# Optimization experiments

Measured on AMD Instinct MI355X. Metric: run time of the kernel, lower is better.

The kernel has to match this reference:

```python
import jax, jax.numpy as jnp
import numpy as np

EMB_SIZE = 768
BLOCK_SIZE = 64
OFFSET = 1  # bert cls offset


def setup_inputs() -> dict:
    key = jax.random.key(0)
    ks = jax.random.split(key, 10)
    n, c, d, h, E, M, P = 4, 1024, 768, 12, 42, 8, 1024
    sequence_output = jax.random.normal(ks[0], (n, c, d), jnp.float32)
    attention = jax.random.uniform(ks[1], (n, h, c, c), jnp.float32)
    attention = attention / attention.sum(-1, keepdims=True)  # softmax-like rows
    Wh = jax.random.normal(ks[2], (EMB_SIZE, 2 * d), jnp.float32) * 0.02
    bh = jax.random.normal(ks[3], (EMB_SIZE,), jnp.float32) * 0.02
    Wt = jax.random.normal(ks[4], (EMB_SIZE, 2 * d), jnp.float32) * 0.02
    bt = jax.random.normal(ks[5], (EMB_SIZE,), jnp.float32) * 0.02
    Wb = jax.random.normal(ks[6], (99, EMB_SIZE * BLOCK_SIZE), jnp.float32) * 0.02
    mention_pos = jax.random.randint(ks[7], (n, E, M), 0, c - 1 - OFFSET, jnp.int32)
    mention_mask = jax.random.randint(ks[8], (n, E, M), 0, 2, jnp.int32)
    mention_mask = mention_mask.at[:, :, 0].set(1)  # every entity has >=1 mention
    hts = jax.random.randint(ks[9], (n, P, 2), 0, E, jnp.int32)
    return {"sequence_output": sequence_output, "attention": attention,
            "Wh": Wh, "bh": bh, "Wt": Wt, "bt": bt, "Wb": Wb,
            "mention_pos": mention_pos, "mention_mask": mention_mask, "hts": hts}


def _get_hrt_doc(seq, att, pos, mask, ht):
    # seq [c,d], att [h,c,c], pos/mask [E,M], ht [P,2]
    p = pos + OFFSET                                   # [E,M]
    valid = mask > 0
    memb = seq[p]                                      # [E,M,d] gather
    e_emb = jax.scipy.special.logsumexp(
        jnp.where(valid[..., None], memb, -jnp.inf), axis=1)  # [E,d]
    matt = att[:, p]                                   # [h,E,M,c] gather
    cnt = valid.sum(1).astype(seq.dtype)               # [E]
    e_att = (matt * valid[None, :, :, None].astype(seq.dtype)).sum(2)
    e_att = jnp.transpose(e_att, (1, 0, 2)) / cnt[:, None, None]  # [E,h,c] mention mean
    hs = e_emb[ht[:, 0]]                               # [P,d]
    ts = e_emb[ht[:, 1]]
    h_att = e_att[ht[:, 0]]                            # [P,h,c]
    t_att = e_att[ht[:, 1]]
    ht_att = (h_att * t_att).mean(1)                   # [P,c] head mean
    ht_att = ht_att / (ht_att.sum(1, keepdims=True) + 1e-5)
    rs = jnp.einsum('ld,rl->rd', seq, ht_att)          # [P,d]
    return hs, ts, rs


def reference(sequence_output, attention, Wh, bh, Wt, bt, Wb,
              mention_pos, mention_mask, hts):
    d = sequence_output.shape[-1]
    hs, ts, rs = jax.vmap(_get_hrt_doc)(sequence_output, attention,
                                        mention_pos, mention_mask, hts)
    hs = hs.reshape(-1, d)
    ts = ts.reshape(-1, d)
    rs = rs.reshape(-1, d)
    hs = jnp.tanh(jnp.concatenate([hs, rs], axis=1) @ Wh.T + bh)
    ts = jnp.tanh(jnp.concatenate([ts, rs], axis=1) @ Wt.T + bt)
    nb = EMB_SIZE // BLOCK_SIZE
    b1 = hs.reshape(-1, nb, BLOCK_SIZE)
    b2 = ts.reshape(-1, nb, BLOCK_SIZE)
    bl = (b1[:, :, :, None] * b2[:, :, None, :]).reshape(-1, EMB_SIZE * BLOCK_SIZE)
    logits = bl @ Wb.T                                 # [N, num_labels+2]
    return logits
```

## Files before the change

### kernel.cpp

```cpp
#include <hip/hip_runtime.h>
#include <hip/hip_bf16.h>
#include <hip/hip_fp16.h>
#include <math.h>

#define NDOC 4
#define CCC  1024
#define DDD  768
#define HHH  12
#define EEE  42
#define MMM  8
#define PPP  1024
#define NK   99
#define NPAD 112
#define NSLICE 96

typedef __attribute__((ext_vector_type(8))) short short8v;
typedef __attribute__((ext_vector_type(8))) _Float16 half8;
typedef __attribute__((ext_vector_type(4))) float floatx4;

__device__ __forceinline__ unsigned short f32_to_bf16u(float f) {
  return __builtin_bit_cast(unsigned short, __float2bfloat16(f));
}
__device__ __forceinline__ unsigned short f32_to_f16u(float f) {
  return __builtin_bit_cast(unsigned short, __float2half(f));
}

__global__ __launch_bounds__(256) void k_prep(
    const float* __restrict__ seq, const float* __restrict__ att,
    const float* __restrict__ Wh, const float* __restrict__ Wt,
    const float* __restrict__ Wb,
    const int* __restrict__ pos, const int* __restrict__ mask,
    unsigned short* __restrict__ eembB, float* __restrict__ eatt,
    unsigned short* __restrict__ WhtB, unsigned short* __restrict__ seqTB,
    unsigned short* __restrict__ WpB) {
  const int bx = blockIdx.x;
  const int tid = threadIdx.x;
  if (bx < 168) {
    int e = bx % EEE, doc = bx / EEE;
    int base = (doc*EEE + e)*MMM;
    int p[MMM], mk[MMM];
#pragma unroll
    for (int m = 0; m < MMM; ++m) { p[m] = pos[base+m] + 1; mk[m] = mask[base+m]; }
    for (int d0 = tid; d0 < DDD; d0 += 256) {
      float v[MMM]; float mx = -INFINITY;
#pragma unroll
      for (int m = 0; m < MMM; ++m) {
        v[m] = seq[(doc*CCC + p[m])*DDD + d0];
        if (mk[m]) mx = fmaxf(mx, v[m]);
      }
      float s = 0.f;
#pragma unroll
      for (int m = 0; m < MMM; ++m) if (mk[m]) s += expf(v[m]-mx);
      eembB[(doc*EEE + e)*DDD + d0] = f32_to_bf16u(logf(s) + mx);
    }
  } else if (bx < 2184) {
    int b = bx - 168;
    int head = b % HHH, e = (b/HHH) % EEE, doc = b / (HHH*EEE);
    int base = (doc*EEE + e)*MMM;
    int j = tid * 4;
    float ax=0.f, ay=0.f, az=0.f, aw=0.f; float cnt = 0.f;
#pragma unroll
    for (int m = 0; m < MMM; ++m) {
      int mk = mask[base+m];
      cnt += (float)mk;
      if (mk) {
        int pp = pos[base+m] + 1;
        const float4 a = *(const float4*)&att[((size_t)(doc*HHH + head)*CCC + pp)*CCC + j];
        ax += a.x; ay += a.y; az += a.z; aw += a.w;
      }
    }
    float inv = 1.f / cnt;
    float4 o; o.x = ax*inv; o.y = ay*inv; o.z = az*inv; o.w = aw*inv;
    *(float4*)&eatt[((size_t)((doc*EEE + e)*HHH + head))*CCC + j] = o;
  } else if (bx < 3336) {
    int gid = (bx - 2184)*256 + tid;
    int half = gid >= 147456;
    int loc = half ? gid - 147456 : gid;
    const float* src = (half ? Wt : Wh) + (size_t)loc*8;
    float4 v0 = *(const float4*)src;
    float4 v1 = *(const float4*)(src+4);
    unsigned short o[8];
    o[0]=f32_to_bf16u(v0.x); o[1]=f32_to_bf16u(v0.y); o[2]=f32_to_bf16u(v0.z); o[3]=f32_to_bf16u(v0.w);
    o[4]=f32_to_bf16u(v1.x); o[5]=f32_to_bf16u(v1.y); o[6]=f32_to_bf16u(v1.z); o[7]=f32_to_bf16u(v1.w);
    *(uint4*)&WhtB[(size_t)half*1179648 + (size_t)loc*8] = *(const uint4*)o;
  } else if (bx < 4104) {
    __shared__ float tl[64][65];
    int b = bx - 3336;
    int d0 = (b % 12)*64, c0 = ((b/12) % 16)*64, doc = b / 192;
#pragma unroll
    for (int rep = 0; rep < 4; ++rep) {
      int cr = rep*16 + (tid >> 4);
      int d4 = (tid & 15) * 4;
      float4 v = *(const float4*)&seq[((size_t)doc*CCC + c0 + cr)*DDD + d0 + d4];
      tl[cr][d4+0]=v.x; tl[cr][d4+1]=v.y; tl[cr][d4+2]=v.z; tl[cr][d4+3]=v.w;
    }
    __syncthreads();
#pragma unroll
    for (int rep = 0; rep < 4; ++rep) {
      int dr = rep*16 + (tid >> 4);
      int c4 = (tid & 15) * 4;
      unsigned short o[4];
#pragma unroll
      for (int kq = 0; kq < 4; ++kq)
        o[kq] = f32_to_bf16u(tl[c4+kq][dr]);
      *(uint2*)&seqTB[((size_t)doc*DDD + d0 + dr)*CCC + c0 + c4] = *(const uint2*)o;
    }
  } else {
    int t = (bx - 4104)*256 + tid;
    int n  = t / 6144;
    int rem = t % 6144;
    int ki = rem >> 3;
    int j8 = (rem & 7) * 8;
    unsigned short o[8];
    if (n < NK) {
      const float* src = &Wb[(size_t)n*49152 + ki*64 + j8];
      float4 v0 = *(const float4*)src;
      float4 v1 = *(const float4*)(src+4);
      o[0]=f32_to_f16u(v0.x); o[1]=f32_to_f16u(v0.y); o[2]=f32_to_f16u(v0.z); o[3]=f32_to_f16u(v0.w);
      o[4]=f32_to_f16u(v1.x); o[5]=f32_to_f16u(v1.y); o[6]=f32_to_f16u(v1.z); o[7]=f32_to_f16u(v1.w);
    } else {
#pragma unroll
      for (int e=0;e<8;++e) o[e]=0;
    }
    int js = j8 >> 5, q = (j8 >> 3) & 3;
    int nt = n >> 4, lnn = n & 15;
    int c = ((js*7 + nt)*4 + q)*16 + lnn;
    *(uint4*)&WpB[(size_t)ki*7168 + c*8] = *(const uint4*)o;
  }
}

__global__ __launch_bounds__(256) void k_htatt1(const float* __restrict__ eatt,
    const int* __restrict__ hts, float* __restrict__ htU,
    float* __restrict__ Ssum) {
  __shared__ float tile[EEE*16*12];
  const int cg = blockIdx.x, doc = blockIdx.y;
  const int c0 = cg * 16;
  for (int idx = threadIdx.x; idx < EEE*16*12; idx += 256) {
    int e = idx / 192, rem = idx % 192, h = rem / 16, cc = rem % 16;
    tile[(e*16 + cc)*12 + h] =
        eatt[((size_t)((doc*EEE + e)*HHH + h))*CCC + c0 + cc];
  }
  __syncthreads();
  const int cc = threadIdx.x & 15;
  const int pg = threadIdx.x >> 4;
  for (int it = 0; it < 64; ++it) {
    int p = pg + it*16;
    int h0 = hts[(doc*PPP + p)*2 + 0];
    int t0 = hts[(doc*PPP + p)*2 + 1];
    const float* a = &tile[(h0*16 + cc)*12];
    const float* b = &tile[(t0*16 + cc)*12];
    float4 a0 = *(const float4*)a,     b0 = *(const float4*)b;
    float4 a1 = *(const float4*)(a+4), b1 = *(const float4*)(b+4);
    float4 a2 = *(const float4*)(a+8), b2 = *(const float4*)(b+8);
    float s = a0.x*b0.x + a0.y*b0.y + a0.z*b0.z + a0.w*b0.w
            + a1.x*b1.x + a1.y*b1.y + a1.z*b1.z + a1.w*b1.w
            + a2.x*b2.x + a2.y*b2.y + a2.z*b2.z + a2.w*b2.w;
    s *= (1.f/12.f);
    htU[((size_t)(doc*PPP + p))*CCC + c0 + cc] = s;
    float r = s;
    r += __shfl_xor(r, 1, 16);
    r += __shfl_xor(r, 2, 16);
    r += __shfl_xor(r, 4, 16);
    r += __shfl_xor(r, 8, 16);
    if (cc == 0) Ssum[((size_t)(doc*PPP + p))*64 + cg] = r;
  }
}

__global__ __launch_bounds__(256) void k_htnorm(const float* __restrict__ htU,
    const float* __restrict__ Ssum, unsigned short* __restrict__ htB) {
  __shared__ float sc_sh;
  const int b = blockIdx.x;
  const int lane = threadIdx.x;
  if (lane < 64) {
    float r = Ssum[(size_t)b*64 + lane];
    for (int off = 32; off > 0; off >>= 1) r += __shfl_down(r, off, 64);
    if (lane == 0) sc_sh = 1.f / (r + 1e-5f);
  }
  __syncthreads();
  float sc = sc_sh;
  float4 v = *(const float4*)&htU[(size_t)b*CCC + lane*4];
  unsigned short o[4];
  o[0] = f32_to_bf16u(v.x*sc); o[1] = f32_to_bf16u(v.y*sc);
  o[2] = f32_to_bf16u(v.z*sc); o[3] = f32_to_bf16u(v.w*sc);
  *(uint2*)&htB[(size_t)b*CCC + lane*4] = *(const uint2*)o;
}

__global__ __launch_bounds__(256) void k_rs_mfma(
    const unsigned short* __restrict__ htB,
    const unsigned short* __restrict__ seqTB,
    unsigned short* __restrict__ rsB) {
  __shared__ unsigned short A_l[4096];
  __shared__ unsigned short B_l[4096];
  const int n0 = blockIdx.x * 128;
  const int m0 = blockIdx.y * 128;
  const int doc = m0 >> 10;
  const int mloc = m0 & 1023;
  const int t = threadIdx.x;
  const int lane = t & 63;
  const int ln = lane & 15, q4 = lane >> 4;
  const int w = t >> 6;
  const int wr = w >> 1, wc = w & 1;

  const int r0 = t >> 2;
  const int koff = (t & 3) * 8;
  const unsigned short* srcA0 = htB + ((size_t)doc*CCC + mloc + r0)*CCC + koff;
  const unsigned short* srcA1 = htB + ((size_t)doc*CCC + mloc + r0 + 64)*CCC + koff;
  const unsigned short* srcB0 = seqTB + ((size_t)doc*DDD + n0 + r0)*CCC + koff;
  const unsigned short* srcB1 = seqTB + ((size_t)doc*DDD + n0 + r0 + 64)*CCC + koff;

  floatx4 acc[4][4];
#pragma unroll
  for (int i = 0; i < 4; ++i)
#pragma unroll
    for (int j = 0; j < 4; ++j) acc[i][j] = (floatx4){0.f,0.f,0.f,0.f};

  for (int k0 = 0; k0 < CCC; k0 += 32) {
    uint4 va0 = *(const uint4*)(srcA0 + k0);
    uint4 va1 = *(const uint4*)(srcA1 + k0);
    uint4 vb0 = *(const uint4*)(srcB0 + k0);
    uint4 vb1 = *(const uint4*)(srcB1 + k0);
    __syncthreads();
    *(uint4*)&A_l[(size_t)t*8]       = va0;
    *(uint4*)&A_l[(size_t)(t+256)*8] = va1;
    *(uint4*)&B_l[(size_t)t*8]       = vb0;
    *(uint4*)&B_l[(size_t)(t+256)*8] = vb1;
    __syncthreads();
    short8v a[4], b[4];
#pragma unroll
    for (int rt = 0; rt < 4; ++rt)
      a[rt] = *(const short8v*)&A_l[((wr*64 + rt*16 + ln)*4 + q4)*8];
#pragma unroll
    for (int nt = 0; nt < 4; ++nt)
      b[nt] = *(const short8v*)&B_l[((wc*64 + nt*16 + ln)*4 + q4)*8];
#pragma unroll
    for (int rt = 0; rt < 4; ++rt)
#pragma unroll
      for (int nt = 0; nt < 4; ++nt)
        acc[rt][nt] = __builtin_amdgcn_mfma_f32_16x16x32_bf16(a[rt], b[nt], acc[rt][nt], 0, 0, 0);
  }
#pragma unroll
  for (int rt = 0; rt < 4; ++rt)
#pragma unroll
    for (int nt = 0; nt < 4; ++nt) {
      int col = n0 + wc*64 + nt*16 + ln;
#pragma unroll
      for (int reg = 0; reg < 4; ++reg) {
        int row = m0 + wr*64 + rt*16 + q4*4 + reg;
        rsB[(size_t)row*DDD + col] = f32_to_bf16u(acc[rt][nt][reg]);
      }
    }
}

__global__ __launch_bounds__(256) void k_heads_mfma(
    const unsigned short* __restrict__ eembB,
    const unsigned short* __restrict__ rsB,
    const int* __restrict__ hts,
    const unsigned short* __restrict__ WB,
    const float* __restrict__ bh, const float* __restrict__ bt,
    unsigned short* __restrict__ hsTB,
    unsigned short* __restrict__ tsbH) {
  __shared__ unsigned short A_l[4096];
  __shared__ unsigned short B_l[4096];
  __shared__ unsigned short T_l[128*144];
  const int which = blockIdx.z;
  const int n0 = blockIdx.x * 128;
  const int m0 = blockIdx.y * 128;
  const int doc = m0 >> 10;
  const int t = threadIdx.x;
  const int lane = t & 63;
  const int ln = lane & 15, q4 = lane >> 4;
  const int w = t >> 6;
  const int wr = w >> 1, wc = w & 1;

  const int r0 = t >> 2;
  const int koff = (t & 3) * 8;
  const int rgA0 = m0 + r0, rgA1 = m0 + r0 + 64;
  const int idx0 = hts[rgA0*2 + which];
  const int idx1 = hts[rgA1*2 + which];
  const unsigned short* srcE0 = eembB + (size_t)(doc*EEE + idx0)*DDD + koff;
  const unsigned short* srcE1 = eembB + (size_t)(doc*EEE + idx1)*DDD + koff;
  const unsigned short* srcR0 = rsB + (size_t)rgA0*DDD + koff;
  const unsigned short* srcR1 = rsB + (size_t)rgA1*DDD + koff;
  const unsigned short* WBz = WB + (size_t)which*1179648;
  const unsigned short* srcW0 = WBz + (size_t)(n0 + r0)*1536 + koff;
  const unsigned short* srcW1 = WBz + (size_t)(n0 + r0 + 64)*1536 + koff;

  floatx4 acc[4][4];
#pragma unroll
  for (int i = 0; i < 4; ++i)
#pragma unroll
    for (int j = 0; j < 4; ++j) acc[i][j] = (floatx4){0.f,0.f,0.f,0.f};

  for (int k0 = 0; k0 < 1536; k0 += 32) {
    uint4 va0 = (k0 < DDD) ? *(const uint4*)(srcE0 + k0) : *(const uint4*)(srcR0 + (k0 - DDD));
    uint4 va1 = (k0 < DDD) ? *(const uint4*)(srcE1 + k0) : *(const uint4*)(srcR1 + (k0 - DDD));
    uint4 vb0 = *(const uint4*)(srcW0 + k0);
    uint4 vb1 = *(const uint4*)(srcW1 + k0);
    __syncthreads();
    *(uint4*)&A_l[(size_t)t*8]       = va0;
    *(uint4*)&A_l[(size_t)(t+256)*8] = va1;
    *(uint4*)&B_l[(size_t)t*8]       = vb0;
    *(uint4*)&B_l[(size_t)(t+256)*8] = vb1;
    __syncthreads();
    short8v a[4], b[4];
#pragma unroll
    for (int rt = 0; rt < 4; ++rt)
      a[rt] = *(const short8v*)&A_l[((wr*64 + rt*16 + ln)*4 + q4)*8];
#pragma unroll
    for (int nt = 0; nt < 4; ++nt)
      b[nt] = *(const short8v*)&B_l[((wc*64 + nt*16 + ln)*4 + q4)*8];
#pragma unroll
    for (int rt = 0; rt < 4; ++rt)
#pragma unroll
      for (int nt = 0; nt < 4; ++nt)
        acc[rt][nt] = __builtin_amdgcn_mfma_f32_16x16x32_bf16(a[rt], b[nt], acc[rt][nt], 0, 0, 0);
  }
  const float* bias = which ? bt : bh;
  if (which == 0) {
#pragma unroll
    for (int rt = 0; rt < 4; ++rt)
#pragma unroll
      for (int nt = 0; nt < 4; ++nt) {
        int col = wc*64 + nt*16 + ln;
        float bsv = bias[n0 + col];
#pragma unroll
        for (int reg = 0; reg < 4; ++reg) {
          int row = wr*64 + rt*16 + q4*4 + reg;
          T_l[col*144 + row] = f32_to_f16u(tanhf(acc[rt][nt][reg] + bsv));
        }
      }
    __syncthreads();
#pragma unroll
    for (int iter = 0; iter < 8; ++iter) {
      int col = iter*16 + (t >> 4);
      int rblk = t & 15;
      uint4 v = *(const uint4*)&T_l[col*144 + rblk*8];
      *(uint4*)&hsTB[(size_t)(n0 + col)*4096 + m0 + rblk*8] = v;
    }
  } else {
#pragma unroll
    for (int rt = 0; rt < 4; ++rt)
#pragma unroll
      for (int nt = 0; nt < 4; ++nt) {
        int col = n0 + wc*64 + nt*16 + ln;
        float bsv = bias[col];
#pragma unroll
        for (int reg = 0; reg < 4; ++reg) {
          int row = m0 + wr*64 + rt*16 + q4*4 + reg;
          tsbH[(size_t)row*DDD + col] = f32_to_f16u(tanhf(acc[rt][nt][reg] + bsv));
        }
      }
  }
}

__global__ __launch_bounds__(128) void k_logits_mfma(
    const unsigned short* __restrict__ hsT,
    const unsigned short* __restrict__ tsbH,
    const unsigned short* __restrict__ Wp,
    unsigned short* __restrict__ P) {
  __shared__ unsigned short hsT_l[8*128];
  const int slice = blockIdx.x;
  const int kbase = slice * 8;
  const int nb = slice >> 3;
  const int mtile = blockIdx.y;
  const int t = threadIdx.x;
  const int w = t >> 6;
  const int lane = t & 63;
  const int ln = lane & 15;
  const int q = lane >> 4;
  const int m0w = mtile*128 + w*64;

  {
    int ii = t >> 4;
    int c8 = (t & 15) * 8;
    uint4 v = *(const uint4*)&hsT[(size_t)(kbase + ii)*4096 + mtile*128 + c8];
    *(uint4*)&hsT_l[ii*128 + c8] = v;
  }

  __half2 tsr2[4][2][4];
#pragma unroll
  for (int rt = 0; rt < 4; ++rt) {
    int row = m0w + rt*16 + ln;
#pragma unroll
    for (int js = 0; js < 2; ++js) {
      uint4 v = *(const uint4*)&tsbH[(size_t)row*DDD + nb*64 + js*32 + q*8];
      tsr2[rt][js][0] = __builtin_bit_cast(__half2, v.x);
      tsr2[rt][js][1] = __builtin_bit_cast(__half2, v.y);
      tsr2[rt][js][2] = __builtin_bit_cast(__half2, v.z);
      tsr2[rt][js][3] = __builtin_bit_cast(__half2, v.w);
    }
  }

  floatx4 acc[4][7];
#pragma unroll
  for (int rt = 0; rt < 4; ++rt)
#pragma unroll
    for (int nt = 0; nt < 7; ++nt)
      acc[rt][nt] = (floatx4){0.f,0.f,0.f,0.f};

  __syncthreads();

  const unsigned short* wb = Wp + (size_t)kbase*7168;
#pragma unroll
  for (int ii = 0; ii < 8; ++ii) {
    __half2 hh[4];
#pragma unroll
    for (int rt = 0; rt < 4; ++rt) {
      unsigned short hb = hsT_l[ii*128 + w*64 + rt*16 + ln];
      hh[rt] = __half2half2(__ushort_as_half(hb));
    }
#pragma unroll
    for (int js = 0; js < 2; ++js) {
      half8 b[7];
#pragma unroll
      for (int nt = 0; nt < 7; ++nt)
        b[nt] = __builtin_bit_cast(half8,
            *(const uint4*)&wb[((size_t)ii*896 + (js*7 + nt)*64 + lane)*8]);
      half8 a[4];
#pragma unroll
      for (int rt = 0; rt < 4; ++rt) {
        uint4 au;
        au.x = __builtin_bit_cast(unsigned int, __hmul2(hh[rt], tsr2[rt][js][0]));
        au.y = __builtin_bit_cast(unsigned int, __hmul2(hh[rt], tsr2[rt][js][1]));
        au.z = __builtin_bit_cast(unsigned int, __hmul2(hh[rt], tsr2[rt][js][2]));
        au.w = __builtin_bit_cast(unsigned int, __hmul2(hh[rt], tsr2[rt][js][3]));
        a[rt] = __builtin_bit_cast(half8, au);
      }
#pragma unroll
      for (int nt = 0; nt < 7; ++nt)
#pragma unroll
        for (int rt = 0; rt < 4; ++rt)
          acc[rt][nt] = __builtin_amdgcn_mfma_f32_16x16x32_f16(a[rt], b[nt], acc[rt][nt], 0, 0, 0);
    }
  }

  unsigned short* Ps = P + (size_t)slice*(4096*NPAD);
#pragma unroll
  for (int nt = 0; nt < 7; ++nt) {
    int col = nt*16 + ln;
#pragma unroll
    for (int rt = 0; rt < 4; ++rt) {
#pragma unroll
      for (int reg = 0; reg < 4; ++reg) {
        int row = m0w + rt*16 + q*4 + reg;
        Ps[(size_t)row*NPAD + col] = f32_to_f16u(acc[rt][nt][reg]);
      }
    }
  }
}

__global__ __launch_bounds__(256) void k_logred(const unsigned short* __restrict__ P,
    float* __restrict__ out) {
  int idx = blockIdx.x*256 + threadIdx.x;
  int r = idx / NPAD;
  int c = idx % NPAD;
  if (c >= NK) return;
  float s = 0.f;
#pragma unroll 8
  for (int sl = 0; sl < NSLICE; ++sl)
    s += __half2float(__ushort_as_half(P[(size_t)sl*(4096*NPAD) + idx]));
  out[(size_t)r*NK + c] = s;
}

extern "C" void kernel_launch(void* const* d_in, const int* in_sizes, int n_in,
                              void* d_out, int out_size, void* d_ws, size_t ws_size,
                              hipStream_t stream) {
  const float* seq  = (const float*)d_in[0];
  const float* att  = (const float*)d_in[1];
  const float* Wh   = (const float*)d_in[2];
  const float* bh   = (const float*)d_in[3];
  const float* Wt   = (const float*)d_in[4];
  const float* bt   = (const float*)d_in[5];
  const float* Wb   = (const float*)d_in[6];
  const int* pos    = (const int*)d_in[7];
  const int* mask   = (const int*)d_in[8];
  const int* hts    = (const int*)d_in[9];
  float* out = (float*)d_out;

  float* ws = (float*)d_ws;
  float*          eatt  = ws;
  float*          htU   = ws + 2064384;
  float*          Ssum  = ws + 6258688;
  unsigned short* htB   = (unsigned short*)(ws + 6520832);
  unsigned short* eembB = (unsigned short*)(ws + 8617984);
  unsigned short* seqTB = (unsigned short*)(ws + 8682496);
  unsigned short* WhtB  = (unsigned short*)(ws + 10255360);
  unsigned short* rsB   = (unsigned short*)(ws + 11435008);
  unsigned short* hsTB  = (unsigned short*)(ws + 13007872);
  unsigned short* tsbH  = (unsigned short*)(ws + 14580736);
  unsigned short* WpB   = (unsigned short*)(ws + 16153600);
  unsigned short* Pp    = (unsigned short*)(ws + 18906112);

  k_prep<<<dim3(6792), 256, 0, stream>>>(seq, att, Wh, Wt, Wb, pos, mask,
                                         eembB, eatt, WhtB, seqTB, WpB);
  k_htatt1<<<dim3(64, NDOC), 256, 0, stream>>>(eatt, hts, htU, Ssum);
  k_htnorm<<<dim3(NDOC*PPP), 256, 0, stream>>>(htU, Ssum, htB);
  k_rs_mfma<<<dim3(6, 32), 256, 0, stream>>>(htB, seqTB, rsB);
  k_heads_mfma<<<dim3(6, 32, 2), 256, 0, stream>>>(eembB, rsB, hts, WhtB, bh, bt, hsTB, tsbH);
  k_logits_mfma<<<dim3(NSLICE, 32), 128, 0, stream>>>(hsTB, tsbH, WpB, Pp);
  k_logred<<<dim3(4096*NPAD/256), 256, 0, stream>>>(Pp, out);
}
```

Measured before the change: 257.8 us.

## Restructure logits kernel: larger tiles, LDS-staged weights with register prefetch, XCD swizzle

The logits MFMA kernel now has each 256-thread block cover 256 rows and 16 k-slices, halving the slice count and the partial-sum traffic into the reduction. Weight tiles are staged cooperatively into shared memory, with the next tile prefetched into registers while the current one is used. Block indices are remapped so neighbouring work groups land on the same XCD. Partial outputs are written with nontemporal stores. The costs are extra barriers, more register pressure and more LDS use per block.

```diff
diff --git a/kernel.cpp b/kernel.cpp
--- a/kernel.cpp
+++ b/kernel.cpp
@@ -12,7 +12,7 @@
 #define PPP  1024
 #define NK   99
 #define NPAD 112
-#define NSLICE 96
+#define NSLICE 48
 
 typedef __attribute__((ext_vector_type(8))) short short8v;
 typedef __attribute__((ext_vector_type(8))) _Float16 half8;
@@ -353,28 +353,33 @@
   }
 }
 
-__global__ __launch_bounds__(128) void k_logits_mfma(
+__global__ __launch_bounds__(256) void k_logits_mfma(
     const unsigned short* __restrict__ hsT,
     const unsigned short* __restrict__ tsbH,
     const unsigned short* __restrict__ Wp,
     unsigned short* __restrict__ P) {
-  __shared__ unsigned short hsT_l[8*128];
-  const int slice = blockIdx.x;
-  const int kbase = slice * 8;
-  const int nb = slice >> 3;
-  const int mtile = blockIdx.y;
+  __shared__ unsigned short hsT_l[16*256];
+  __shared__ unsigned short slab[2*7168];
+  const int bid = blockIdx.x;
+  const int wg = (bid & 7)*96 + (bid >> 3);
+  const int slice = wg >> 4;
+  const int mgroup = wg & 15;
+  const int kbase = slice * 16;
+  const int nb = kbase >> 6;
   const int t = threadIdx.x;
   const int w = t >> 6;
   const int lane = t & 63;
   const int ln = lane & 15;
   const int q = lane >> 4;
-  const int m0w = mtile*128 + w*64;
-
-  {
-    int ii = t >> 4;
-    int c8 = (t & 15) * 8;
-    uint4 v = *(const uint4*)&hsT[(size_t)(kbase + ii)*4096 + mtile*128 + c8];
-    *(uint4*)&hsT_l[ii*128 + c8] = v;
+  const int m0w = mgroup*256 + w*64;
+
+#pragma unroll
+  for (int rep = 0; rep < 2; ++rep) {
+    int c16 = t + rep*256;
+    int ii = c16 >> 5;
+    int c8 = (c16 & 31) * 8;
+    uint4 v = *(const uint4*)&hsT[(size_t)(kbase + ii)*4096 + mgroup*256 + c8];
+    *(uint4*)&hsT_l[ii*256 + c8] = v;
   }
 
   __half2 tsr2[4][2][4];
@@ -398,39 +403,61 @@
     for (int nt = 0; nt < 7; ++nt)
       acc[rt][nt] = (floatx4){0.f,0.f,0.f,0.f};
 
+  uint4 wreg[7];
+#pragma unroll
+  for (int r = 0; r < 7; ++r)
+    wreg[r] = *(const uint4*)&Wp[(size_t)kbase*7168 + (t + r*256)*8];
+#pragma unroll
+  for (int r = 0; r < 7; ++r)
+    *(uint4*)&slab[(t + r*256)*8] = wreg[r];
   __syncthreads();
 
-  const unsigned short* wb = Wp + (size_t)kbase*7168;
-#pragma unroll
-  for (int ii = 0; ii < 8; ++ii) {
-    __half2 hh[4];
-#pragma unroll
-    for (int rt = 0; rt < 4; ++rt) {
-      unsigned short hb = hsT_l[ii*128 + w*64 + rt*16 + ln];
-      hh[rt] = __half2half2(__ushort_as_half(hb));
-    }
-#pragma unroll
-    for (int js = 0; js < 2; ++js) {
-      half8 b[7];
-#pragma unroll
-      for (int nt = 0; nt < 7; ++nt)
-        b[nt] = __builtin_bit_cast(half8,
-            *(const uint4*)&wb[((size_t)ii*896 + (js*7 + nt)*64 + lane)*8]);
-      half8 a[4];
+  for (int ks = 0; ks < 8; ++ks) {
+    if (ks < 7) {
+      int kin = kbase + (ks + 1)*2;
+#pragma unroll
+      for (int r = 0; r < 7; ++r)
+        wreg[r] = *(const uint4*)&Wp[(size_t)kin*7168 + (t + r*256)*8];
+    }
+#pragma unroll
+    for (int il = 0; il < 2; ++il) {
+      int ii = ks*2 + il;
+      __half2 hh[4];
 #pragma unroll
       for (int rt = 0; rt < 4; ++rt) {
-        uint4 au;
-        au.x = __builtin_bit_cast(unsigned int, __hmul2(hh[rt], tsr2[rt][js][0]));
-        au.y = __builtin_bit_cast(unsigned int, __hmul2(hh[rt], tsr2[rt][js][1]));
-        au.z = __builtin_bit_cast(unsigned int, __hmul2(hh[rt], tsr2[rt][js][2]));
-        au.w = __builtin_bit_cast(unsigned int, __hmul2(hh[rt], tsr2[rt][js][3]));
-        a[rt] = __builtin_bit_cast(half8, au);
-      }
-#pragma unroll
-      for (int nt = 0; nt < 7; ++nt)
-#pragma unroll
-        for (int rt = 0; rt < 4; ++rt)
-          acc[rt][nt] = __builtin_amdgcn_mfma_f32_16x16x32_f16(a[rt], b[nt], acc[rt][nt], 0, 0, 0);
+        unsigned short hb = hsT_l[ii*256 + w*64 + rt*16 + ln];
+        hh[rt] = __half2half2(__ushort_as_half(hb));
+      }
+#pragma unroll
+      for (int js = 0; js < 2; ++js) {
+        half8 b[7];
+#pragma unroll
+        for (int nt = 0; nt < 7; ++nt)
+          b[nt] = __builtin_bit_cast(half8,
+              *(const short8v*)&slab[((size_t)il*896 + (js*7 + nt)*64 + lane)*8]);
+        half8 a[4];
+#pragma unroll
+        for (int rt = 0; rt < 4; ++rt) {
+          uint4 au;
+          au.x = __builtin_bit_cast(unsigned int, __hmul2(hh[rt], tsr2[rt][js][0]));
+          au.y = __builtin_bit_cast(unsigned int, __hmul2(hh[rt], tsr2[rt][js][1]));
+          au.z = __builtin_bit_cast(unsigned int, __hmul2(hh[rt], tsr2[rt][js][2]));
+          au.w = __builtin_bit_cast(unsigned int, __hmul2(hh[rt], tsr2[rt][js][3]));
+          a[rt] = __builtin_bit_cast(half8, au);
+        }
+#pragma unroll
+        for (int nt = 0; nt < 7; ++nt)
+#pragma unroll
+          for (int rt = 0; rt < 4; ++rt)
+            acc[rt][nt] = __builtin_amdgcn_mfma_f32_16x16x32_f16(a[rt], b[nt], acc[rt][nt], 0, 0, 0);
+      }
+    }
+    if (ks < 7) {
+      __syncthreads();
+#pragma unroll
+      for (int r = 0; r < 7; ++r)
+        *(uint4*)&slab[(t + r*256)*8] = wreg[r];
+      __syncthreads();
     }
   }
 
@@ -443,7 +470,8 @@
 #pragma unroll
       for (int reg = 0; reg < 4; ++reg) {
         int row = m0w + rt*16 + q*4 + reg;
-        Ps[(size_t)row*NPAD + col] = f32_to_f16u(acc[rt][nt][reg]);
+        __builtin_nontemporal_store(f32_to_f16u(acc[rt][nt][reg]),
+                                    &Ps[(size_t)row*NPAD + col]);
       }
     }
   }
@@ -497,6 +525,6 @@
   k_htnorm<<<dim3(NDOC*PPP), 256, 0, stream>>>(htU, Ssum, htB);
   k_rs_mfma<<<dim3(6, 32), 256, 0, stream>>>(htB, seqTB, rsB);
   k_heads_mfma<<<dim3(6, 32, 2), 256, 0, stream>>>(eembB, rsB, hts, WhtB, bh, bt, hsTB, tsbH);
-  k_logits_mfma<<<dim3(NSLICE, 32), 128, 0, stream>>>(hsTB, tsbH, WpB, Pp);
+  k_logits_mfma<<<dim3(48*16), 256, 0, stream>>>(hsTB, tsbH, WpB, Pp);
   k_logred<<<dim3(4096*NPAD/256), 256, 0, stream>>>(Pp, out);
 }
```

Result: faster. 242.7 us (-5.8%).
